# Kernel tuning notes

Hardware: AMD Instinct MI355X
Metric: run time of the kernel (lower is better)

## Reference

```python
import jax, jax.numpy as jnp
import numpy as np

EPS = 1e-8  # torch F.cosine_similarity eps


def _l2norm(x):
    # x / max(||x||, eps), matching torch cosine_similarity's clamped denominator
    n = jnp.sqrt(jnp.sum(x * x, axis=-1, keepdims=True))
    return x / jnp.maximum(n, EPS)


def setup_inputs() -> dict:
    key = jax.random.key(0)
    k1, k2, k3 = jax.random.split(key, 3)
    B, S, C, D = 16, 512, 16, 512
    return {
        "output": jax.random.normal(k1, (B, C), dtype=jnp.float32),
        "target_text_feats": jax.random.normal(k2, (B, S, C, D), dtype=jnp.float32),
        "vis_feats": jax.random.normal(k3, (B, S, D), dtype=jnp.float32),
    }


def reference(output, target_text_feats, vis_feats):
    B, S, C, D = target_text_feats.shape
    vn = _l2norm(vis_feats)              # (B, S, D)
    tn = _l2norm(target_text_feats)      # (B, S, C, D)
    # sim[b,p,v,t] = cos(vis[b,v], text[b,t,p]); replaces the per-prompt python loop
    sim = jnp.einsum('bvd,btpd->bpvt', vn, tn)  # (B, C, S, S)
    diag = jnp.diagonal(sim, axis1=-2, axis2=-1)      # (B, C, S): sim[b,p,i,i]
    lse_row = jax.nn.logsumexp(sim, axis=-1)          # CE over text axis (logits_per_image)
    lse_col = jax.nn.logsumexp(sim, axis=-2)          # CE over vis axis  (logits_per_text)
    # per-sample clip loss, averaged over the v axis -> (B, C)
    clip_loss = jnp.mean(0.5 * (lse_row + lse_col) - diag, axis=-1)
    clip_loss = jax.lax.stop_gradient(clip_loss)      # computed under torch.no_grad()

    loss = jnp.mean(jnp.square(output - clip_loss))

    gt_labels = jnp.argmin(clip_loss, axis=-1)        # (B,)
    preds = jnp.argmin(output, axis=-1)               # (B,)
    acc = jnp.mean((preds == gt_labels).astype(jnp.float32)) * 100.0
    prompt_id_preds = jnp.broadcast_to(preds[:, None, None], (B, S, 1))
    return loss, acc, prompt_id_preds
```

## Files before the change

kernel.cpp:

```cpp
#include <hip/hip_runtime.h>

#define EPSN 1e-8f

typedef _Float16 half8 __attribute__((ext_vector_type(8)));
typedef __fp16 fp16x2 __attribute__((ext_vector_type(2)));
typedef float floatx4 __attribute__((ext_vector_type(4)));

#define LDS_BARRIER()                                              \
    do {                                                           \
        asm volatile("s_waitcnt lgkmcnt(0)" ::: "memory");         \
        __builtin_amdgcn_s_barrier();                              \
        asm volatile("" ::: "memory");                             \
    } while (0)

__global__ __launch_bounds__(256) void k_vinv(const float* __restrict__ vis,
                                              float* __restrict__ vinv) {
    int row  = blockIdx.x * 4 + (threadIdx.x >> 6);
    int lane = threadIdx.x & 63;
    const float4* src = reinterpret_cast<const float4*>(vis + (size_t)row * 512);
    float4 a = src[lane];
    float4 b = src[lane + 64];
    float s = a.x*a.x + a.y*a.y + a.z*a.z + a.w*a.w
            + b.x*b.x + b.y*b.y + b.z*b.z + b.w*b.w;
    #pragma unroll
    for (int off = 1; off < 64; off <<= 1) s += __shfl_xor(s, off);
    if (lane == 0) vinv[row] = 1.0f / fmaxf(sqrtf(s), EPSN);
}

#define LDA 32

__global__ __launch_bounds__(256, 4) void k_main(
    const float* __restrict__ vis, const float* __restrict__ text,
    const float* __restrict__ vinv,
    float* __restrict__ g_rowsum, float* __restrict__ g_colsum,
    float* __restrict__ g_dsum)
{
    __shared__ _Float16 Ash[128 * LDA];
    __shared__ _Float16 Bsh[128 * LDA];
    __shared__ float tn2[128];
    __shared__ float vinvS[128];
    __shared__ float rowS[128];
    __shared__ float colS[128];

    const int pid = blockIdx.x;
    const int xcd = pid & 7;
    const int s_  = pid >> 3;
    const int blk = (s_ & 3) + (xcd << 2) + ((s_ >> 2) << 5);

    const int vq   = blk & 3;
    const int tb   = (blk >> 2) & 3;
    const int bp   = blk >> 4;
    const int p    = bp & 15;
    const int b    = bp >> 4;
    const int tid  = threadIdx.x;
    const int lane = tid & 63;
    const int wave = tid >> 6;
    const int wy   = wave >> 1;
    const int wx   = wave & 1;
    const int m15  = lane & 15;
    const int g4   = lane >> 4;

    if (tid < 128) {
        rowS[tid] = 0.f; colS[tid] = 0.f;
        vinvS[tid] = vinv[b * 512 + vq * 128 + tid];
    }

    floatx4 acc[4][4];
    floatx4 zf = {0.f, 0.f, 0.f, 0.f};
    #pragma unroll
    for (int mb = 0; mb < 4; ++mb)
        #pragma unroll
        for (int nb = 0; nb < 4; ++nb) acc[mb][nb] = zf;

    const int srow = tid >> 1;
    const int sko  = (tid & 1) * 16;
    const int xw  = (srow >> 1) & 3;
    const int s0  = (tid & 1) * 2;
    const int wo0 = srow * LDA + (((s0)     ^ xw) << 3);
    const int wo1 = srow * LDA + (((s0 + 1) ^ xw) << 3);
    const int koff = ((g4 ^ ((m15 >> 1) & 3)) << 3);

    const float* aPtr =
        vis + (size_t)b * 512 * 512 + (size_t)(vq * 128 + srow) * 512 + sko;
    const float* bPtr =
        text + ((size_t)((b * 512 + tb * 128 + srow) * 16 + p)) * 512 + sko;

    float tsq = 0.f;

    for (int kc = 0; kc < 16; ++kc) {
        float4 a0 = *reinterpret_cast<const float4*>(aPtr);
        float4 a1 = *reinterpret_cast<const float4*>(aPtr + 4);
        float4 a2 = *reinterpret_cast<const float4*>(aPtr + 8);
        float4 a3 = *reinterpret_cast<const float4*>(aPtr + 12);
        float4 b0 = *reinterpret_cast<const float4*>(bPtr);
        float4 b1 = *reinterpret_cast<const float4*>(bPtr + 4);
        float4 b2 = *reinterpret_cast<const float4*>(bPtr + 8);
        float4 b3 = *reinterpret_cast<const float4*>(bPtr + 12);
        aPtr += 32; bPtr += 32;

        {
            union { half8 v; fp16x2 q[4]; } u;
            u.q[0] = __builtin_amdgcn_cvt_pkrtz(a0.x, a0.y);
            u.q[1] = __builtin_amdgcn_cvt_pkrtz(a0.z, a0.w);
            u.q[2] = __builtin_amdgcn_cvt_pkrtz(a1.x, a1.y);
            u.q[3] = __builtin_amdgcn_cvt_pkrtz(a1.z, a1.w);
            *reinterpret_cast<half8*>(&Ash[wo0]) = u.v;
            u.q[0] = __builtin_amdgcn_cvt_pkrtz(a2.x, a2.y);
            u.q[1] = __builtin_amdgcn_cvt_pkrtz(a2.z, a2.w);
            u.q[2] = __builtin_amdgcn_cvt_pkrtz(a3.x, a3.y);
            u.q[3] = __builtin_amdgcn_cvt_pkrtz(a3.z, a3.w);
            *reinterpret_cast<half8*>(&Ash[wo1]) = u.v;
        }
        tsq += b0.x*b0.x + b0.y*b0.y + b0.z*b0.z + b0.w*b0.w
             + b1.x*b1.x + b1.y*b1.y + b1.z*b1.z + b1.w*b1.w
             + b2.x*b2.x + b2.y*b2.y + b2.z*b2.z + b2.w*b2.w
             + b3.x*b3.x + b3.y*b3.y + b3.z*b3.z + b3.w*b3.w;
        {
            union { half8 v; fp16x2 q[4]; } u;
            u.q[0] = __builtin_amdgcn_cvt_pkrtz(b0.x, b0.y);
            u.q[1] = __builtin_amdgcn_cvt_pkrtz(b0.z, b0.w);
            u.q[2] = __builtin_amdgcn_cvt_pkrtz(b1.x, b1.y);
            u.q[3] = __builtin_amdgcn_cvt_pkrtz(b1.z, b1.w);
            *reinterpret_cast<half8*>(&Bsh[wo0]) = u.v;
            u.q[0] = __builtin_amdgcn_cvt_pkrtz(b2.x, b2.y);
            u.q[1] = __builtin_amdgcn_cvt_pkrtz(b2.z, b2.w);
            u.q[2] = __builtin_amdgcn_cvt_pkrtz(b3.x, b3.y);
            u.q[3] = __builtin_amdgcn_cvt_pkrtz(b3.z, b3.w);
            *reinterpret_cast<half8*>(&Bsh[wo1]) = u.v;
        }
        LDS_BARRIER();
        half8 af[4];
        #pragma unroll
        for (int mb = 0; mb < 4; ++mb)
            af[mb] = *reinterpret_cast<const half8*>(
                &Ash[(wy * 64 + mb * 16 + m15) * LDA + koff]);
        #pragma unroll
        for (int nb = 0; nb < 4; ++nb) {
            half8 bf = *reinterpret_cast<const half8*>(
                &Bsh[(wx * 64 + nb * 16 + m15) * LDA + koff]);
            #pragma unroll
            for (int mb = 0; mb < 4; ++mb)
                acc[mb][nb] = __builtin_amdgcn_mfma_f32_16x16x32_f16(
                    af[mb], bf, acc[mb][nb], 0, 0, 0);
        }
        LDS_BARRIER();
    }

    tsq += __shfl_xor(tsq, 1);
    if ((tid & 1) == 0)
        tn2[srow] = 1.0f / fmaxf(sqrtf(tsq), EPSN);
    __syncthreads();

    float tinvc[4];
    #pragma unroll
    for (int nb = 0; nb < 4; ++nb) tinvc[nb] = tn2[wx * 64 + nb * 16 + m15];

    float colpart[4];
    #pragma unroll
    for (int nb = 0; nb < 4; ++nb) colpart[nb] = 0.f;
    float dsum = 0.f;

    #pragma unroll
    for (int mb = 0; mb < 4; ++mb) {
        #pragma unroll
        for (int r = 0; r < 4; ++r) {
            int vloc  = wy * 64 + mb * 16 + g4 * 4 + r;
            int vglob = vq * 128 + vloc;
            float vi  = vinvS[vloc];
            float rp  = 0.f;
            #pragma unroll
            for (int nb = 0; nb < 4; ++nb) {
                float sim  = acc[mb][nb][r] * vi * tinvc[nb];
                int tglob  = tb * 128 + wx * 64 + nb * 16 + m15;
                if (vglob == tglob) dsum += sim;
                float e = __expf(sim);
                rp += e;
                colpart[nb] += e;
            }
            rp += __shfl_xor(rp, 1);
            rp += __shfl_xor(rp, 2);
            rp += __shfl_xor(rp, 4);
            rp += __shfl_xor(rp, 8);
            if (m15 == 0) atomicAdd(&rowS[vloc], rp);
        }
    }
    #pragma unroll
    for (int nb = 0; nb < 4; ++nb) {
        float cp = colpart[nb];
        cp += __shfl_xor(cp, 16);
        cp += __shfl_xor(cp, 32);
        if (lane < 16) atomicAdd(&colS[wx * 64 + nb * 16 + lane], cp);
    }
    if (vq == tb) {
        #pragma unroll
        for (int off = 1; off < 64; off <<= 1) dsum += __shfl_xor(dsum, off);
        if (lane == 0) atomicAdd(&g_dsum[bp], dsum);
    }
    __syncthreads();
    if (tid < 128) {
        atomicAdd(&g_rowsum[(size_t)bp * 512 + vq * 128 + tid], rowS[tid]);
        atomicAdd(&g_colsum[(size_t)bp * 512 + tb * 128 + tid], colS[tid]);
    }
}

__global__ __launch_bounds__(256) void k_clip(
    const float* __restrict__ g_rowsum, const float* __restrict__ g_colsum,
    const float* __restrict__ g_dsum, float* __restrict__ clip)
{
    __shared__ float red[4];
    int bp = blockIdx.x, tid = threadIdx.x;
    int lane = tid & 63, wave = tid >> 6;
    float s = 0.f;
    #pragma unroll
    for (int c = 0; c < 2; ++c) {
        int i = c * 256 + tid;
        s += 0.5f * (logf(g_rowsum[(size_t)bp * 512 + i]) +
                     logf(g_colsum[(size_t)bp * 512 + i]));
    }
    #pragma unroll
    for (int off = 1; off < 64; off <<= 1) s += __shfl_xor(s, off);
    if (lane == 0) red[wave] = s;
    __syncthreads();
    if (tid == 0)
        clip[bp] = (red[0] + red[1] + red[2] + red[3] - g_dsum[bp]) * (1.0f / 512.0f);
}

__global__ __launch_bounds__(256) void k_final(
    const float* __restrict__ clip, const float* __restrict__ output,
    float* __restrict__ out)
{
    __shared__ float cl[256], ou[256], red[4];
    __shared__ int preds[16];
    int tid = threadIdx.x, lane = tid & 63, wave = tid >> 6;
    cl[tid] = clip[tid];
    ou[tid] = output[tid];
    __syncthreads();
    float d = ou[tid] - cl[tid];
    float s = d * d;
    #pragma unroll
    for (int off = 1; off < 64; off <<= 1) s += __shfl_xor(s, off);
    if (lane == 0) red[wave] = s;
    if (tid < 16) {
        float m = ou[tid * 16]; int a = 0;
        for (int q = 1; q < 16; ++q)
            if (ou[tid * 16 + q] < m) { m = ou[tid * 16 + q]; a = q; }
        preds[tid] = a;
    }
    __syncthreads();
    if (tid == 0) {
        int cnt = 0;
        for (int bb = 0; bb < 16; ++bb) {
            float m = cl[bb * 16]; int a = 0;
            for (int q = 1; q < 16; ++q)
                if (cl[bb * 16 + q] < m) { m = cl[bb * 16 + q]; a = q; }
            cnt += (preds[bb] == a);
        }
        out[0] = (red[0] + red[1] + red[2] + red[3]) * (1.0f / 256.0f);
        out[1] = (float)cnt * (100.0f / 16.0f);
    }
    __syncthreads();
    for (int j = tid; j < 16 * 512; j += 256)
        out[2 + j] = (float)preds[j >> 9];
}

extern "C" void kernel_launch(void* const* d_in, const int* in_sizes, int n_in,
                              void* d_out, int out_size, void* d_ws, size_t ws_size,
                              hipStream_t stream)
{
    const float* output = (const float*)d_in[0];
    const float* text   = (const float*)d_in[1];
    const float* vis    = (const float*)d_in[2];

    float* g_rowsum = (float*)d_ws;
    float* g_colsum = g_rowsum + 256 * 512;
    float* g_dsum   = g_colsum + 256 * 512;
    float* clip     = g_dsum + 256;
    float* vinv     = clip + 256;
    (void)hipMemsetAsync(d_ws, 0, (size_t)(2 * 256 * 512 + 256) * sizeof(float), stream);

    k_vinv <<<2048, 256, 0, stream>>>(vis, vinv);
    k_main <<<4096, 256, 0, stream>>>(vis, text, vinv, g_rowsum, g_colsum, g_dsum);
    k_clip <<<256, 256, 0, stream>>>(g_rowsum, g_colsum, g_dsum, clip);
    k_final<<<1, 256, 0, stream>>>(clip, output, (float*)d_out);
}
```

Baseline: 477.0 us.

## Pre-normalize inputs to fp16 and stream tiles via global_load_lds

Adds a prep kernel that L2-normalizes vis and text rows, converts them to fp16, and writes text transposed to a (B,C,S,D) layout in workspace. The main GEMM kernel then loads pre-converted fp16 tiles straight into swizzled LDS with global_load_lds, which drops per-tile conversion and norm work inside the hot loop. It keeps the legacy path as a fallback when the workspace is too small. The cost is an extra full pass over the 268MB text tensor plus a 134MB fp16 write, and main still rereads the fp16 copy four times. Whether this pays off depends on how much the old kernel was bound by in-loop conversion rather than by memory traffic.

```diff
diff --git a/kernel.cpp b/kernel.cpp
--- a/kernel.cpp
+++ b/kernel.cpp
@@ -12,6 +12,172 @@
         __builtin_amdgcn_s_barrier();                              \
         asm volatile("" ::: "memory");                             \
     } while (0)
+
+#define GLL16(g, l)                                                        \
+    __builtin_amdgcn_global_load_lds(                                      \
+        (const __attribute__((address_space(1))) unsigned int*)(g),        \
+        (__attribute__((address_space(3))) unsigned int*)(l), 16, 0, 0)
+
+__global__ __launch_bounds__(256) void k_prep(
+    const float* __restrict__ vis, const float* __restrict__ text,
+    _Float16* __restrict__ visH, _Float16* __restrict__ textH)
+{
+    int row  = blockIdx.x * 4 + (threadIdx.x >> 6);
+    int lane = threadIdx.x & 63;
+    const float* src;
+    _Float16* dst;
+    if (row < 8192) {
+        src = vis + (size_t)row * 512;
+        dst = visH + (size_t)row * 512;
+    } else {
+        int r  = row - 8192;
+        int c  = r & 15;
+        int s  = (r >> 4) & 511;
+        int bb = r >> 13;
+        src = text + (size_t)r * 512;
+        dst = textH + ((size_t)(bb * 16 + c) * 512 + s) * 512;
+    }
+    const float4* s4 = reinterpret_cast<const float4*>(src);
+    float4 x = s4[lane * 2];
+    float4 y = s4[lane * 2 + 1];
+    float ss = x.x*x.x + x.y*x.y + x.z*x.z + x.w*x.w
+             + y.x*y.x + y.y*y.y + y.z*y.z + y.w*y.w;
+    #pragma unroll
+    for (int off = 1; off < 64; off <<= 1) ss += __shfl_xor(ss, off);
+    float rinv = 1.0f / fmaxf(sqrtf(ss), EPSN);
+    union { half8 v; fp16x2 q[4]; } u;
+    u.q[0] = __builtin_amdgcn_cvt_pkrtz(x.x * rinv, x.y * rinv);
+    u.q[1] = __builtin_amdgcn_cvt_pkrtz(x.z * rinv, x.w * rinv);
+    u.q[2] = __builtin_amdgcn_cvt_pkrtz(y.x * rinv, y.y * rinv);
+    u.q[3] = __builtin_amdgcn_cvt_pkrtz(y.z * rinv, y.w * rinv);
+    *reinterpret_cast<half8*>(dst + lane * 8) = u.v;
+}
+
+__global__ __launch_bounds__(256, 4) void k_main(
+    const _Float16* __restrict__ visH, const _Float16* __restrict__ textH,
+    float* __restrict__ g_rowsum, float* __restrict__ g_colsum,
+    float* __restrict__ g_dsum)
+{
+    __shared__ _Float16 Ash[128 * 64];
+    __shared__ _Float16 Bsh[128 * 64];
+    __shared__ float rowS[128];
+    __shared__ float colS[128];
+
+    const int pid = blockIdx.x;
+    const int xcd = pid & 7;
+    const int s_  = pid >> 3;
+    const int blk = (s_ & 3) + (xcd << 2) + ((s_ >> 2) << 5);
+
+    const int vq   = blk & 3;
+    const int tb   = (blk >> 2) & 3;
+    const int bp   = blk >> 4;
+    const int b    = bp >> 4;
+    const int tid  = threadIdx.x;
+    const int lane = tid & 63;
+    const int wave = tid >> 6;
+    const int wy   = wave >> 1;
+    const int wx   = wave & 1;
+    const int m15  = lane & 15;
+    const int g4   = lane >> 4;
+
+    if (tid < 128) { rowS[tid] = 0.f; colS[tid] = 0.f; }
+
+    floatx4 acc[4][4];
+    floatx4 zf = {0.f, 0.f, 0.f, 0.f};
+    #pragma unroll
+    for (int mb = 0; mb < 4; ++mb)
+        #pragma unroll
+        for (int nb = 0; nb < 4; ++nb) acc[mb][nb] = zf;
+
+    const int w32 = wave * 32;
+    const int lr8 = lane >> 3;
+    const int ls  = lane & 7;
+    const int swz = ls ^ lr8;
+    const _Float16* aSrc =
+        visH + ((size_t)(b * 512 + vq * 128 + w32 + lr8)) * 512 + swz * 8;
+    const _Float16* bSrc =
+        textH + ((size_t)(bp * 512 + tb * 128 + w32 + lr8)) * 512 + swz * 8;
+    _Float16* aDst = &Ash[w32 * 64];
+    _Float16* bDst = &Bsh[w32 * 64];
+
+    for (int kc = 0; kc < 8; ++kc) {
+        const int ko = kc * 64;
+        #pragma unroll
+        for (int i = 0; i < 4; ++i) {
+            GLL16(aSrc + i * (8 * 512) + ko, aDst + i * 512);
+            GLL16(bSrc + i * (8 * 512) + ko, bDst + i * 512);
+        }
+        asm volatile("s_waitcnt vmcnt(0)" ::: "memory");
+        __builtin_amdgcn_s_barrier();
+        asm volatile("" ::: "memory");
+        #pragma unroll
+        for (int ki = 0; ki < 2; ++ki) {
+            half8 af[4];
+            #pragma unroll
+            for (int mb = 0; mb < 4; ++mb)
+                af[mb] = *reinterpret_cast<const half8*>(
+                    &Ash[(wy * 64 + mb * 16 + m15) * 64 +
+                         (((ki * 4 + g4) ^ (m15 & 7)) * 8)]);
+            #pragma unroll
+            for (int nb = 0; nb < 4; ++nb) {
+                half8 bf = *reinterpret_cast<const half8*>(
+                    &Bsh[(wx * 64 + nb * 16 + m15) * 64 +
+                         (((ki * 4 + g4) ^ (m15 & 7)) * 8)]);
+                #pragma unroll
+                for (int mb = 0; mb < 4; ++mb)
+                    acc[mb][nb] = __builtin_amdgcn_mfma_f32_16x16x32_f16(
+                        af[mb], bf, acc[mb][nb], 0, 0, 0);
+            }
+        }
+        LDS_BARRIER();
+    }
+
+    float colpart[4];
+    #pragma unroll
+    for (int nb = 0; nb < 4; ++nb) colpart[nb] = 0.f;
+    float dsum = 0.f;
+
+    #pragma unroll
+    for (int mb = 0; mb < 4; ++mb) {
+        #pragma unroll
+        for (int r = 0; r < 4; ++r) {
+            int vloc  = wy * 64 + mb * 16 + g4 * 4 + r;
+            int vglob = vq * 128 + vloc;
+            float rp  = 0.f;
+            #pragma unroll
+            for (int nb = 0; nb < 4; ++nb) {
+                float sim  = acc[mb][nb][r];
+                int tglob  = tb * 128 + wx * 64 + nb * 16 + m15;
+                if (vglob == tglob) dsum += sim;
+                float e = __expf(sim);
+                rp += e;
+                colpart[nb] += e;
+            }
+            rp += __shfl_xor(rp, 1);
+            rp += __shfl_xor(rp, 2);
+            rp += __shfl_xor(rp, 4);
+            rp += __shfl_xor(rp, 8);
+            if (m15 == 0) atomicAdd(&rowS[vloc], rp);
+        }
+    }
+    #pragma unroll
+    for (int nb = 0; nb < 4; ++nb) {
+        float cp = colpart[nb];
+        cp += __shfl_xor(cp, 16);
+        cp += __shfl_xor(cp, 32);
+        if (lane < 16) atomicAdd(&colS[wx * 64 + nb * 16 + lane], cp);
+    }
+    if (vq == tb) {
+        #pragma unroll
+        for (int off = 1; off < 64; off <<= 1) dsum += __shfl_xor(dsum, off);
+        if (lane == 0) atomicAdd(&g_dsum[bp], dsum);
+    }
+    __syncthreads();
+    if (tid < 128) {
+        atomicAdd(&g_rowsum[(size_t)bp * 512 + vq * 128 + tid], rowS[tid]);
+        atomicAdd(&g_colsum[(size_t)bp * 512 + tb * 128 + tid], colS[tid]);
+    }
+}
 
 __global__ __launch_bounds__(256) void k_vinv(const float* __restrict__ vis,
                                               float* __restrict__ vinv) {
@@ -29,7 +195,7 @@
 
 #define LDA 32
 
-__global__ __launch_bounds__(256, 4) void k_main(
+__global__ __launch_bounds__(256, 4) void k_main_legacy(
     const float* __restrict__ vis, const float* __restrict__ text,
     const float* __restrict__ vinv,
     float* __restrict__ g_rowsum, float* __restrict__ g_colsum,
@@ -276,10 +442,20 @@
     float* g_dsum   = g_colsum + 256 * 512;
     float* clip     = g_dsum + 256;
     float* vinv     = clip + 256;
+    _Float16* visH  = (_Float16*)(vinv + 8192);
+    _Float16* textH = visH + (size_t)8192 * 512;
+    size_t need = (size_t)((char*)(textH + (size_t)131072 * 512) - (char*)d_ws);
+
     (void)hipMemsetAsync(d_ws, 0, (size_t)(2 * 256 * 512 + 256) * sizeof(float), stream);
 
-    k_vinv <<<2048, 256, 0, stream>>>(vis, vinv);
-    k_main <<<4096, 256, 0, stream>>>(vis, text, vinv, g_rowsum, g_colsum, g_dsum);
+    if (ws_size >= need) {
+        k_prep<<<(8192 + 131072) / 4, 256, 0, stream>>>(vis, text, visH, textH);
+        k_main<<<4096, 256, 0, stream>>>(visH, textH, g_rowsum, g_colsum, g_dsum);
+    } else {
+        k_vinv<<<2048, 256, 0, stream>>>(vis, vinv);
+        k_main_legacy<<<4096, 256, 0, stream>>>(vis, text, vinv,
+                                                g_rowsum, g_colsum, g_dsum);
+    }
     k_clip <<<256, 256, 0, stream>>>(g_rowsum, g_colsum, g_dsum, clip);
     k_final<<<1, 256, 0, stream>>>(clip, output, (float*)d_out);
 }
```

Result: no change. 485.3 us (+1.7%).
